# Kernel tuning notes

Measured on AMD Instinct MI355X. Metric: run time of the kernel, lower is better.

Reference implementation:

```python
import jax, jax.numpy as jnp
import numpy as np

D = 1024
EPS = 1e-5  # torch LayerNorm default


def setup_inputs() -> dict:
    key = jax.random.key(0)
    ks = jax.random.split(key, 10)
    B, S = 4, 2048
    s = 1.0 / np.sqrt(D)
    inp = {
        "x": jax.random.normal(ks[0], (B, S, D), dtype=jnp.float32),
        "gamma": jnp.ones((D,), jnp.float32),
        "beta": jnp.zeros((D,), jnp.float32),
        "Wq": jax.random.normal(ks[1], (D, D), jnp.float32) * s,
        "bq": jax.random.normal(ks[2], (D,), jnp.float32) * 0.01,
        "Wk": jax.random.normal(ks[3], (D, D), jnp.float32) * s,
        "bk": jax.random.normal(ks[4], (D,), jnp.float32) * 0.01,
        "Wv": jax.random.normal(ks[5], (D, D), jnp.float32) * s,
        "bv": jax.random.normal(ks[6], (D,), jnp.float32) * 0.01,
        "Wo": jax.random.normal(ks[7], (D, D), jnp.float32) * s,
        "bo": jax.random.normal(ks[8], (D,), jnp.float32) * 0.01,
    }
    return inp


def reference(x, gamma, beta, Wq, bq, Wk, bk, Wv, bv, Wo, bo):
    # Pre-LayerNorm
    mu = jnp.mean(x, axis=-1, keepdims=True)
    var = jnp.mean(jnp.square(x - mu), axis=-1, keepdims=True)
    xn = (x - mu) * jax.lax.rsqrt(var + EPS) * gamma + beta
    # QKV projections (torch Linear: y = x @ W.T + b)
    Q = jnp.einsum('bsd,ed->bse', xn, Wq) + bq
    K = jnp.einsum('bsd,ed->bse', xn, Wk) + bk
    V = jnp.einsum('bsd,ed->bse', xn, Wv) + bv
    # Single-head full attention, scaled by sqrt(D); dropout inactive (eval)
    scores = jnp.einsum('bqd,bkd->bqk', Q, K) / jnp.sqrt(jnp.float32(D))
    attn = jax.nn.softmax(scores, axis=-1)
    out = jnp.einsum('bqk,bkd->bqd', attn, V)
    return jnp.einsum('bsd,ed->bse', out, Wo) + bo
```

## Files before the change

kernel.cpp:

```cpp
#include <hip/hip_runtime.h>
#include <hip/hip_bf16.h>
#include <stdint.h>

typedef __attribute__((ext_vector_type(4))) float f32x4;
typedef __attribute__((ext_vector_type(8))) __bf16 bf16x8;
typedef __attribute__((ext_vector_type(8))) unsigned short ushort8;

#define DEV static __device__ __forceinline__

__device__ __align__(4096) unsigned char g_scratch[96600064];

DEV unsigned short f2bf(float f) {
  union { float f; uint32_t u; } x; x.f = f;
  uint32_t u = x.u;
  uint32_t r = (u + 0x7fffu + ((u >> 16) & 1u)) >> 16;
  return (unsigned short)r;
}
DEV float bf2f(unsigned short b) {
  union { uint32_t u; float f; } x; x.u = ((uint32_t)b) << 16;
  return x.f;
}

DEV void gload16(const void* g, void* l) {
  __builtin_amdgcn_global_load_lds((const __attribute__((address_space(1))) void*)g,
                                   (__attribute__((address_space(3))) void*)l,
                                   16, 0, 0);
}

DEV int swz(int b) { return b ^ (((b >> 7) & 7) << 4); }

DEV void gemm_core(const unsigned short* a_t, const unsigned short* b_t,
                   int ldA, int ldB, int K, unsigned short* lds, int tid,
                   const int* aOff, const int* bOff, f32x4 acc[4][4])
{
  for (int kt = 0; kt < K; kt += 64) {
#pragma unroll
    for (int i = 0; i < 4; ++i) {
      int o = i * 4096 + tid * 16;
      int p = swz(o);
      int row = p >> 7;
      int ce  = (p & 127) >> 1;
      gload16(a_t + (size_t)row * ldA + (kt + ce), (char*)lds + o);
      gload16(b_t + (size_t)row * ldB + (kt + ce), (char*)lds + 16384 + o);
    }
    __syncthreads();
#pragma unroll
    for (int h = 0; h < 2; ++h) {
      bf16x8 av[4], bv4[4];
#pragma unroll
      for (int m = 0; m < 4; ++m)
        av[m] = *(const bf16x8*)((const char*)lds + (aOff[m] ^ (h << 6)));
#pragma unroll
      for (int n = 0; n < 4; ++n)
        bv4[n] = *(const bf16x8*)((const char*)lds + (bOff[n] ^ (h << 6)));
#pragma unroll
      for (int m = 0; m < 4; ++m)
#pragma unroll
        for (int n = 0; n < 4; ++n)
          acc[m][n] = __builtin_amdgcn_mfma_f32_16x16x32_bf16(av[m], bv4[n], acc[m][n], 0, 0, 0);
    }
    __syncthreads();
  }
}

DEV void frag_offsets(int lane, int wm, int wn, int* aOff, int* bOff)
{
#pragma unroll
  for (int m = 0; m < 4; ++m) {
    int ar = wm + m * 16 + (lane & 15);
    aOff[m] = (ar * 128 + ((lane >> 4) * 16)) ^ ((ar & 7) << 4);
    int br = wn + m * 16 + (lane & 15);
    bOff[m] = ((br * 128 + ((lane >> 4) * 16)) ^ ((br & 7) << 4)) + 16384;
  }
}

DEV void tile_readback(const char* lb, unsigned short* dst, size_t ldC,
                       int wave, int lane)
{
#pragma unroll
  for (int j = 0; j < 8; ++j) {
    int row_l = wave * 32 + (lane >> 4) * 8 + j;
    int byte = (row_l * 256 + (lane & 15) * 16) ^ ((row_l & 12) << 3);
    ushort8 v = *(const ushort8*)(lb + byte);
    *(ushort8*)(dst + (size_t)row_l * ldC + (lane & 15) * 8) = v;
  }
}

__global__ __launch_bounds__(256, 4)
void g0(const unsigned short* __restrict__ wkT, const unsigned short* __restrict__ wqT,
        const unsigned short* __restrict__ woB, const unsigned short* __restrict__ wvT,
        unsigned short* __restrict__ mt, unsigned short* __restrict__ w4,
        const float* __restrict__ bq, const float* __restrict__ Wo,
        const float* __restrict__ bv, const float* __restrict__ bo,
        float* __restrict__ cvec, float* __restrict__ bb, float* __restrict__ rsm,
        const float* __restrict__ x, const float* __restrict__ gamma,
        const float* __restrict__ beta, unsigned short* __restrict__ xn)
{
  __shared__ unsigned short lds[16384];
  const int bid = blockIdx.x;
  const int tid = threadIdx.x, lane = tid & 63, wave = tid >> 6;

  if (bid >= 640) {
    const int row = bid - 640;
    float* red1 = (float*)lds;
    float* red2 = (float*)lds + 4;
    const float4 xv = ((const float4*)(x + (size_t)row * 1024))[tid];
    float s = xv.x + xv.y + xv.z + xv.w;
#pragma unroll
    for (int d = 1; d < 64; d <<= 1) s += __shfl_xor(s, d);
    if (lane == 0) red1[wave] = s;
    __syncthreads();
    const float mu = (red1[0] + red1[1] + red1[2] + red1[3]) * (1.0f / 1024.0f);
    float4 dv;
    dv.x = xv.x - mu; dv.y = xv.y - mu; dv.z = xv.z - mu; dv.w = xv.w - mu;
    float vs = dv.x * dv.x + dv.y * dv.y + dv.z * dv.z + dv.w * dv.w;
#pragma unroll
    for (int d = 1; d < 64; d <<= 1) vs += __shfl_xor(vs, d);
    if (lane == 0) red2[wave] = vs;
    __syncthreads();
    const float var = (red2[0] + red2[1] + red2[2] + red2[3]) * (1.0f / 1024.0f);
    const float rs = rsqrtf(var + 1e-5f);
    const float4 g = ((const float4*)gamma)[tid];
    const float4 b = ((const float4*)beta)[tid];
    ushort4 o;
    o.x = f2bf(dv.x * rs * g.x + b.x);
    o.y = f2bf(dv.y * rs * g.y + b.y);
    o.z = f2bf(dv.z * rs * g.z + b.z);
    o.w = f2bf(dv.w * rs * g.w + b.w);
    ((ushort4*)(xn + (size_t)row * 1024))[tid] = o;
    return;
  }

  if (bid >= 128) {
    const int b2 = bid - 128;
    if (b2 < 256) {
      if (b2 < 4) {
        const int i2 = (b2 * 256 + tid) * 2;
        ((float4*)rsm)[i2] = make_float4(0.f, 0.f, 0.f, 0.f);
        ((float4*)rsm)[i2 + 1] = make_float4(0.f, 0.f, 0.f, 0.f);
      }
      const int d = b2 * 4 + wave;
      float s = 0.f;
#pragma unroll
      for (int q = 0; q < 2; ++q) {
        ushort8 v = *(const ushort8*)(wkT + (size_t)d * 1024 + lane * 16 + q * 8);
#pragma unroll
        for (int k = 0; k < 8; ++k)
          s += bf2f(v[k]) * bq[lane * 16 + q * 8 + k];
      }
#pragma unroll
      for (int dd = 1; dd < 64; dd <<= 1) s += __shfl_xor(s, dd);
      if (lane == 0) cvec[d] = s * 0.03125f;
    } else {
      const int e = (b2 - 256) * 4 + wave;
      float s = 0.f;
#pragma unroll
      for (int q = 0; q < 4; ++q) {
        float4 a = *(const float4*)(Wo + (size_t)e * 1024 + lane * 16 + q * 4);
        float4 b = *(const float4*)(bv + lane * 16 + q * 4);
        s += a.x * b.x + a.y * b.y + a.z * b.z + a.w * b.w;
      }
#pragma unroll
      for (int dd = 1; dd < 64; dd <<= 1) s += __shfl_xor(s, dd);
      if (lane == 0) bb[e] = s + bo[e];
    }
    return;
  }

  const int z = bid >> 6;
  const int idx = bid & 63;
  const int m0 = (idx >> 3) * 128, n0 = (idx & 7) * 128;
  const int wm = (wave >> 1) * 64, wn = (wave & 1) * 64;
  int aOff[4], bOff[4];
  frag_offsets(lane, wm, wn, aOff, bOff);
  f32x4 acc[4][4] = {};
  const unsigned short* a_t = (z == 0) ? (wkT + (size_t)m0 * 1024) : (woB + (size_t)m0 * 1024);
  const unsigned short* b_t = (z == 0) ? (wqT + (size_t)n0 * 1024) : (wvT + (size_t)n0 * 1024);
  gemm_core(a_t, b_t, 1024, 1024, 1024, lds, tid, aOff, bOff, acc);

  const int r0 = (lane >> 4) * 4, cL = lane & 15;
  const float scale = (z == 0) ? 0.03125f : 1.0f;
  unsigned short* Cp = (z == 0) ? mt : w4;
#pragma unroll
  for (int n = 0; n < 4; ++n) {
    int colg = n0 + wn + n * 16 + cL;
#pragma unroll
    for (int m = 0; m < 4; ++m) {
      int rowg = m0 + wm + m * 16 + r0;
#pragma unroll
      for (int i = 0; i < 4; ++i)
        Cp[(size_t)(rowg + i) * 1024 + colg] = f2bf(acc[m][n][i] * scale);
    }
  }
}

__global__ __launch_bounds__(256, 4)
void g1(const unsigned short* __restrict__ xn, const unsigned short* __restrict__ mt,
        const unsigned short* __restrict__ w4, unsigned short* __restrict__ Z,
        unsigned short* __restrict__ yt, const float* __restrict__ cvec,
        float* __restrict__ w)
{
  __shared__ unsigned short lds[16384];
  const int tid = threadIdx.x, lane = tid & 63, wave = tid >> 6;
  const int z = blockIdx.z;

  if (z == 2) {
    const int flat = blockIdx.y * 64 + blockIdx.x;
#pragma unroll
    for (int p = 0; p < 4; ++p) {
      const int j = flat * 16 + wave * 4 + p;
      float s = 0.f;
#pragma unroll
      for (int q = 0; q < 2; ++q) {
        ushort8 v = *(const ushort8*)(xn + (size_t)j * 1024 + lane * 16 + q * 8);
#pragma unroll
        for (int k = 0; k < 8; ++k)
          s += bf2f(v[k]) * cvec[lane * 16 + q * 8 + k];
      }
#pragma unroll
      for (int d = 1; d < 64; d <<= 1) s += __shfl_xor(s, d);
      if (lane == 0) w[j] = s;
    }
    return;
  }

  const int m0 = blockIdx.x * 128, n0 = blockIdx.y * 128;
  const int wm = (wave >> 1) * 64, wn = (wave & 1) * 64;
  int aOff[4], bOff[4];
  frag_offsets(lane, wm, wn, aOff, bOff);
  f32x4 acc[4][4] = {};
  const unsigned short* b_t = ((z == 0) ? mt : w4) + (size_t)n0 * 1024;
  gemm_core(xn + (size_t)m0 * 1024, b_t, 1024, 1024, 1024, lds, tid, aOff, bOff, acc);

  const int r0 = (lane >> 4) * 4, cL = lane & 15;
  if (z == 0) {
    char* lb = (char*)lds;
#pragma unroll
    for (int n = 0; n < 4; ++n) {
      int col_l = wn + n * 16 + cL;
#pragma unroll
      for (int m = 0; m < 4; ++m)
#pragma unroll
        for (int i = 0; i < 4; ++i) {
          int row_l = wm + m * 16 + r0 + i;
          int byte = (row_l * 256 + col_l * 2) ^ ((row_l & 12) << 3);
          *(unsigned short*)(lb + byte) = f2bf(acc[m][n][i]);
        }
    }
    __syncthreads();
    tile_readback(lb, Z + (size_t)m0 * 1024 + n0, 1024, wave, lane);
  } else {
#pragma unroll
    for (int n = 0; n < 4; ++n) {
      int colg = n0 + wn + n * 16 + cL;
#pragma unroll
      for (int m = 0; m < 4; ++m) {
        int rowg = m0 + wm + m * 16 + r0;
        int bat = rowg >> 11, sdx = rowg & 2047;
        ushort4 pk;
        pk.x = f2bf(acc[m][n][0]);
        pk.y = f2bf(acc[m][n][1]);
        pk.z = f2bf(acc[m][n][2]);
        pk.w = f2bf(acc[m][n][3]);
        *(ushort4*)(yt + (size_t)bat * 2097152 + (size_t)colg * 2048 + sdx) = pk;
      }
    }
  }
}

__global__ __launch_bounds__(256, 4)
void g2(const unsigned short* __restrict__ Z, const unsigned short* __restrict__ xn,
        unsigned short* __restrict__ S, const float* __restrict__ w,
        float* __restrict__ rsum)
{
  __shared__ unsigned short lds[16384];
  const int tid = threadIdx.x, lane = tid & 63, wave = tid >> 6;
  const int z = blockIdx.z;
  const int m0 = blockIdx.x * 128, n0 = blockIdx.y * 128;
  const int wm = (wave >> 1) * 64, wn = (wave & 1) * 64;
  int aOff[4], bOff[4];
  frag_offsets(lane, wm, wn, aOff, bOff);
  f32x4 acc[4][4] = {};
  gemm_core(Z + (size_t)z * 2097152 + (size_t)m0 * 1024,
            xn + (size_t)z * 2097152 + (size_t)n0 * 1024,
            1024, 1024, 1024, lds, tid, aOff, bOff, acc);

  const int r0 = (lane >> 4) * 4, cL = lane & 15;
  char* lb = (char*)lds;
  float rs[4][4];
#pragma unroll
  for (int m = 0; m < 4; ++m)
#pragma unroll
    for (int i = 0; i < 4; ++i) rs[m][i] = 0.0f;
#pragma unroll
  for (int n = 0; n < 4; ++n) {
    int col_l = wn + n * 16 + cL;
    float wv = w[(size_t)z * 2048 + n0 + col_l];
#pragma unroll
    for (int m = 0; m < 4; ++m) {
#pragma unroll
      for (int i = 0; i < 4; ++i) {
        int row_l = wm + m * 16 + r0 + i;
        float p = __expf(acc[m][n][i] + wv - 12.0f);
        rs[m][i] += p;
        int byte = (row_l * 256 + col_l * 2) ^ ((row_l & 12) << 3);
        *(unsigned short*)(lb + byte) = f2bf(p);
      }
    }
  }
#pragma unroll
  for (int m = 0; m < 4; ++m)
#pragma unroll
    for (int i = 0; i < 4; ++i) {
      float v = rs[m][i];
      v += __shfl_xor(v, 1);
      v += __shfl_xor(v, 2);
      v += __shfl_xor(v, 4);
      v += __shfl_xor(v, 8);
      if (cL == 0)
        atomicAdd(&rsum[(size_t)z * 2048 + m0 + wm + m * 16 + r0 + i], v);
    }
  __syncthreads();
  tile_readback(lb, S + (size_t)z * 4194304 + (size_t)m0 * 2048 + n0, 2048, wave, lane);
}

__global__ __launch_bounds__(256, 4)
void g3(const unsigned short* __restrict__ S, const unsigned short* __restrict__ yt,
        float* __restrict__ out, const float* __restrict__ bb,
        const float* __restrict__ rsum)
{
  __shared__ unsigned short lds[12288];
  const int tid = threadIdx.x, lane = tid & 63, wave = tid >> 6;
  const int z = blockIdx.z;
  const int m0 = blockIdx.x * 64, n0 = blockIdx.y * 128;
  const int wm = (wave >> 1) * 32, wn = (wave & 1) * 64;

  int aOff[2], bOff[4];
#pragma unroll
  for (int m = 0; m < 2; ++m) {
    int ar = wm + m * 16 + (lane & 15);
    aOff[m] = (ar * 128 + ((lane >> 4) * 16)) ^ ((ar & 7) << 4);
  }
#pragma unroll
  for (int n = 0; n < 4; ++n) {
    int br = wn + n * 16 + (lane & 15);
    bOff[n] = ((br * 128 + ((lane >> 4) * 16)) ^ ((br & 7) << 4)) + 8192;
  }

  const unsigned short* a_t = S + (size_t)z * 4194304 + (size_t)m0 * 2048;
  const unsigned short* b_t = yt + (size_t)z * 2097152 + (size_t)n0 * 2048;

  f32x4 acc[2][4] = {};

  for (int kt = 0; kt < 2048; kt += 64) {
#pragma unroll
    for (int i = 0; i < 2; ++i) {
      int rel = i * 4096 + tid * 16;
      int p = swz(rel);
      int row = p >> 7, ce = (p & 127) >> 1;
      gload16(a_t + (size_t)row * 2048 + (kt + ce), (char*)lds + rel);
    }
#pragma unroll
    for (int i = 0; i < 4; ++i) {
      int rel = i * 4096 + tid * 16;
      int p = swz(rel);
      int row = p >> 7, ce = (p & 127) >> 1;
      gload16(b_t + (size_t)row * 2048 + (kt + ce), (char*)lds + 8192 + rel);
    }
    __syncthreads();
#pragma unroll
    for (int h = 0; h < 2; ++h) {
      bf16x8 av[2], bv4[4];
#pragma unroll
      for (int m = 0; m < 2; ++m)
        av[m] = *(const bf16x8*)((const char*)lds + (aOff[m] ^ (h << 6)));
#pragma unroll
      for (int n = 0; n < 4; ++n)
        bv4[n] = *(const bf16x8*)((const char*)lds + (bOff[n] ^ (h << 6)));
#pragma unroll
      for (int m = 0; m < 2; ++m)
#pragma unroll
        for (int n = 0; n < 4; ++n)
          acc[m][n] = __builtin_amdgcn_mfma_f32_16x16x32_bf16(av[m], bv4[n], acc[m][n], 0, 0, 0);
    }
    __syncthreads();
  }

  const int r0 = (lane >> 4) * 4, cL = lane & 15;
  float* Cp = out + (size_t)z * 2097152;
#pragma unroll
  for (int m = 0; m < 2; ++m) {
    int rowg = m0 + wm + m * 16 + r0;
#pragma unroll
    for (int i = 0; i < 4; ++i) {
      float inv = 1.0f / rsum[(size_t)z * 2048 + rowg + i];
#pragma unroll
      for (int n = 0; n < 4; ++n) {
        int colg = n0 + wn + n * 16 + cL;
        Cp[(size_t)(rowg + i) * 1024 + colg] = acc[m][n][i] * inv + bb[colg];
      }
    }
  }
}

__global__ __launch_bounds__(256)
void prep(const float* __restrict__ Wq, const float* __restrict__ Wk,
          const float* __restrict__ Wv, const float* __restrict__ Wo,
          unsigned short* __restrict__ wqT, unsigned short* __restrict__ wkT,
          unsigned short* __restrict__ wvT, unsigned short* __restrict__ woB)
{
  __shared__ float tlds[64][65];
  const int bid = blockIdx.x;
  const int tid = threadIdx.x;

  if (bid < 512) {
    const int idx = (bid * 256 + tid) * 8;
    const float4 a = *(const float4*)(Wo + idx);
    const float4 b = *(const float4*)(Wo + idx + 4);
    ushort4 r0, r1;
    r0.x = f2bf(a.x); r0.y = f2bf(a.y); r0.z = f2bf(a.z); r0.w = f2bf(a.w);
    r1.x = f2bf(b.x); r1.y = f2bf(b.y); r1.z = f2bf(b.z); r1.w = f2bf(b.w);
    *(ushort4*)(woB + idx) = r0;
    *(ushort4*)(woB + idx + 4) = r1;
    return;
  }
  {
    const int t = bid - 512;
    const int mat = t >> 8;
    const int tile = t & 255;
    const int R0 = (tile >> 4) * 64, C0 = (tile & 15) * 64;
    const float* src = (mat == 0) ? Wq : (mat == 1) ? Wk : Wv;
    unsigned short* dst = (mat == 0) ? wqT : (mat == 1) ? wkT : wvT;
#pragma unroll
    for (int p = 0; p < 4; ++p) {
      int r = p * 16 + (tid >> 4);
      int c = (tid & 15) * 4;
      float4 v = *(const float4*)(src + (size_t)(R0 + r) * 1024 + C0 + c);
      tlds[r][c + 0] = v.x; tlds[r][c + 1] = v.y;
      tlds[r][c + 2] = v.z; tlds[r][c + 3] = v.w;
    }
    __syncthreads();
    const int c = tid >> 2;
    const int chunk = tid & 3;
    ushort8 o0, o1;
#pragma unroll
    for (int k = 0; k < 8; ++k)  o0[k] = f2bf(tlds[chunk * 16 + k][c]);
#pragma unroll
    for (int k = 0; k < 8; ++k)  o1[k] = f2bf(tlds[chunk * 16 + 8 + k][c]);
    unsigned short* dp = dst + (size_t)(C0 + c) * 1024 + R0 + chunk * 16;
    *(ushort8*)(dp) = o0;
    *(ushort8*)(dp + 8) = o1;
  }
}

extern "C" void kernel_launch(void* const* d_in, const int* in_sizes, int n_in,
                              void* d_out, int out_size, void* d_ws, size_t ws_size,
                              hipStream_t stream) {
  const float* x     = (const float*)d_in[0];
  const float* gamma = (const float*)d_in[1];
  const float* beta  = (const float*)d_in[2];
  const float* Wq    = (const float*)d_in[3];
  const float* bq    = (const float*)d_in[4];
  const float* Wk    = (const float*)d_in[5];
  const float* Wv    = (const float*)d_in[7];
  const float* bv    = (const float*)d_in[8];
  const float* Wo    = (const float*)d_in[9];
  const float* bo    = (const float*)d_in[10];

  char* ws;
  if (ws_size >= (size_t)96542720) {
    ws = (char*)d_ws;
  } else {
    void* sp = nullptr;
    hipGetSymbolAddress(&sp, HIP_SYMBOL(g_scratch));
    ws = (char*)sp;
  }

  unsigned short* xn  = (unsigned short*)(ws);
  unsigned short* Z   = (unsigned short*)(ws + 16777216);
  unsigned short* yt  = (unsigned short*)(ws + 33554432);
  unsigned short* S   = (unsigned short*)(ws + 50331648);
  unsigned short* wqT = (unsigned short*)(ws + 83886080);
  unsigned short* wkT = (unsigned short*)(ws + 85983232);
  unsigned short* wvT = (unsigned short*)(ws + 88080384);
  unsigned short* woB = (unsigned short*)(ws + 90177536);
  unsigned short* mt  = (unsigned short*)(ws + 92274688);
  unsigned short* w4  = (unsigned short*)(ws + 94371840);
  float*          wv_ = (float*)(ws + 96468992);
  float*          rsm = (float*)(ws + 96501760);
  float*          bb  = (float*)(ws + 96534528);
  float*          cv  = (float*)(ws + 96538624);

  prep<<<1280, 256, 0, stream>>>(Wq, Wk, Wv, Wo, wqT, wkT, wvT, woB);
  g0<<<8832, 256, 0, stream>>>(wkT, wqT, woB, wvT, mt, w4,
                               bq, Wo, bv, bo, cv, bb, rsm,
                               x, gamma, beta, xn);
  g1<<<dim3(64, 8, 3), 256, 0, stream>>>(xn, mt, w4, Z, yt, cv, wv_);
  g2<<<dim3(16, 16, 4), 256, 0, stream>>>(Z, xn, S, wv_, rsm);
  g3<<<dim3(32, 8, 4), 256, 0, stream>>>(S, yt, (float*)d_out, bb, rsm);
}
```

Before: 152.5 us.

## Add 256x256-tile pipelined score GEMM kernel with 128KB LDS

Adds a new score-GEMM kernel that computes 256x256 output tiles with 8 waves per block. It uses 128KB of dynamic LDS, split into double-buffered A and B stages that are issued interleaved with the MFMA phases, and raises wave priority around the MFMA blocks. The aim is more data reuse per byte loaded and better overlap of global-to-LDS loads with matrix math. The exp, row-sum and atomic epilogue is kept the same as before. In exchange, occupancy drops to one block per CU and only 256 blocks are launched, and the old kernel remains as a fallback if the LDS attribute cannot be set.

New measurement: 162.3 us. 6.4% more time.

```diff
diff --git a/kernel.cpp b/kernel.cpp
--- a/kernel.cpp
+++ b/kernel.cpp
@@ -266,6 +266,152 @@
       }
     }
   }
+}
+
+__global__ __launch_bounds__(512, 1)
+void g2f(const unsigned short* __restrict__ Z, const unsigned short* __restrict__ xn,
+         unsigned short* __restrict__ S, const float* __restrict__ w,
+         float* __restrict__ rsum)
+{
+  extern __shared__ char lds[];
+  const int tid  = threadIdx.x;
+  const int lane = tid & 63;
+  const int wave = tid >> 6;
+  const int wr = wave >> 2;
+  const int wc = wave & 3;
+  const int z  = blockIdx.z;
+  const int m0 = blockIdx.x * 256;
+  const int n0 = blockIdx.y * 256;
+  const int K  = 1024, ldA = 1024, ldB = 1024;
+  const unsigned short* a_t = Z  + (size_t)z * 2097152 + (size_t)m0 * ldA;
+  const unsigned short* b_t = xn + (size_t)z * 2097152 + (size_t)n0 * ldB;
+
+  const int so0 = tid * 16;        const int sp0 = swz(so0);
+  const int sr0 = sp0 >> 7, sc0 = (sp0 & 127) >> 1;
+  const int so1 = 8192 + tid * 16; const int sp1 = swz(so1);
+  const int sr1 = sp1 >> 7, sc1 = (sp1 & 127) >> 1;
+
+  int aoff[8];
+#pragma unroll
+  for (int mi = 0; mi < 8; ++mi) {
+    int r = mi * 16 + (lane & 15);
+    aoff[mi] = (r * 128 + ((lane >> 4) * 16)) ^ ((r & 7) << 4);
+  }
+  int boff[4];
+#pragma unroll
+  for (int ni = 0; ni < 4; ++ni) {
+    int r = (wc & 1) * 64 + ni * 16 + (lane & 15);
+    boff[ni] = (r * 128 + ((lane >> 4) * 16)) ^ ((r & 7) << 4);
+  }
+
+  f32x4 acc[8][4] = {};
+
+  auto STAGE = [&](int base, const unsigned short* src, int ld, int kc) {
+    gload16(src + sr0 * ld + kc + sc0, lds + base + so0);
+    gload16(src + sr1 * ld + kc + sc1, lds + base + so1);
+  };
+
+  const int NI = K >> 7;
+  STAGE(32768,  b_t,             ldB, 0);
+  STAGE(49152,  b_t + 128 * ldB, ldB, 0);
+  STAGE(0,      a_t,             ldA, 0);
+  STAGE(16384,  a_t + 128 * ldA, ldA, 0);
+  STAGE(98304,  b_t,             ldB, 64);
+  STAGE(114688, b_t + 128 * ldB, ldB, 64);
+  asm volatile("s_waitcnt vmcnt(4)" ::: "memory");
+  __builtin_amdgcn_s_barrier();
+
+  for (int it = 0; it < NI; ++it) {
+    const int kA1 = it * 128 + 64;
+    int kn  = it * 128 + 128; if (kn  > K - 64) kn  = K - 64;
+    int kn2 = it * 128 + 192; if (kn2 > K - 64) kn2 = K - 64;
+#pragma unroll
+    for (int c = 0; c < 2; ++c) {
+      const char* aB = lds + c * 65536 + wr * 16384;
+      const char* bB = lds + c * 65536 + 32768 + (wc >> 1) * 16384;
+      bf16x8 bfr[4][2];
+#pragma unroll
+      for (int q = 0; q < 4; ++q) {
+        const int p = c * 4 + q;
+        if (q == 0) {
+#pragma unroll
+          for (int ni = 0; ni < 4; ++ni)
+#pragma unroll
+            for (int h = 0; h < 2; ++h)
+              bfr[ni][h] = *(const bf16x8*)(bB + (boff[ni] ^ (h << 6)));
+        }
+        bf16x8 afr[2][2];
+#pragma unroll
+        for (int m2 = 0; m2 < 2; ++m2)
+#pragma unroll
+          for (int h = 0; h < 2; ++h)
+            afr[m2][h] = *(const bf16x8*)(aB + (aoff[q * 2 + m2] ^ (h << 6)));
+        if (p == 0)      STAGE(65536,  a_t,             ldA, kA1);
+        else if (p == 1) STAGE(81920,  a_t + 128 * ldA, ldA, kA1);
+        else if (p == 2) STAGE(32768,  b_t,             ldB, kn);
+        else if (p == 3) STAGE(49152,  b_t + 128 * ldB, ldB, kn);
+        else if (p == 4) STAGE(0,      a_t,             ldA, kn);
+        else if (p == 5) STAGE(16384,  a_t + 128 * ldA, ldA, kn);
+        else if (p == 6) STAGE(98304,  b_t,             ldB, kn2);
+        else             STAGE(114688, b_t + 128 * ldB, ldB, kn2);
+        if (q == 0) asm volatile("s_waitcnt lgkmcnt(8)" ::: "memory");
+        __builtin_amdgcn_s_barrier();
+        asm volatile("s_waitcnt lgkmcnt(0)" ::: "memory");
+        __builtin_amdgcn_s_setprio(1);
+#pragma unroll
+        for (int h = 0; h < 2; ++h)
+#pragma unroll
+          for (int ni = 0; ni < 4; ++ni)
+#pragma unroll
+            for (int m2 = 0; m2 < 2; ++m2)
+              acc[q * 2 + m2][ni] = __builtin_amdgcn_mfma_f32_16x16x32_bf16(
+                  afr[m2][h], bfr[ni][h], acc[q * 2 + m2][ni], 0, 0, 0);
+        __builtin_amdgcn_s_setprio(0);
+        if (q == 3) asm volatile("s_waitcnt vmcnt(4)" ::: "memory");
+        __builtin_amdgcn_s_barrier();
+      }
+    }
+  }
+
+  const int r0 = (lane >> 4) * 4;
+  const int cL = lane & 15;
+  const int wrow = m0 + wr * 128;
+  const int wcol = n0 + wc * 64;
+  unsigned short* Cp = S + (size_t)z * 4194304;
+
+  float rs[8][4];
+#pragma unroll
+  for (int mi = 0; mi < 8; ++mi)
+#pragma unroll
+    for (int i = 0; i < 4; ++i) rs[mi][i] = 0.0f;
+
+#pragma unroll
+  for (int ni = 0; ni < 4; ++ni) {
+    int colg = wcol + ni * 16 + cL;
+    float wv = w[(size_t)z * 2048 + colg];
+#pragma unroll
+    for (int mi = 0; mi < 8; ++mi) {
+      int rowg = wrow + mi * 16 + r0;
+#pragma unroll
+      for (int i = 0; i < 4; ++i) {
+        float p = __expf(acc[mi][ni][i] + wv - 12.0f);
+        rs[mi][i] += p;
+        Cp[(size_t)(rowg + i) * 2048 + colg] = f2bf(p);
+      }
+    }
+  }
+#pragma unroll
+  for (int mi = 0; mi < 8; ++mi)
+#pragma unroll
+    for (int i = 0; i < 4; ++i) {
+      float v = rs[mi][i];
+      v += __shfl_xor(v, 1);
+      v += __shfl_xor(v, 2);
+      v += __shfl_xor(v, 4);
+      v += __shfl_xor(v, 8);
+      if (cL == 0)
+        atomicAdd(&rsum[(size_t)z * 2048 + wrow + mi * 16 + r0 + i], v);
+    }
 }
 
 __global__ __launch_bounds__(256, 4)
@@ -491,11 +637,19 @@
   float*          bb  = (float*)(ws + 96534528);
   float*          cv  = (float*)(ws + 96538624);
 
+  int use256 =
+      (hipFuncSetAttribute(reinterpret_cast<const void*>(&g2f),
+                           hipFuncAttributeMaxDynamicSharedMemorySize,
+                           131072) == hipSuccess);
+
   prep<<<1280, 256, 0, stream>>>(Wq, Wk, Wv, Wo, wqT, wkT, wvT, woB);
   g0<<<8832, 256, 0, stream>>>(wkT, wqT, woB, wvT, mt, w4,
                                bq, Wo, bv, bo, cv, bb, rsm,
                                x, gamma, beta, xn);
   g1<<<dim3(64, 8, 3), 256, 0, stream>>>(xn, mt, w4, Z, yt, cv, wv_);
-  g2<<<dim3(16, 16, 4), 256, 0, stream>>>(Z, xn, S, wv_, rsm);
+  if (use256)
+    g2f<<<dim3(8, 8, 4), 512, 131072, stream>>>(Z, xn, S, wv_, rsm);
+  else
+    g2<<<dim3(16, 16, 4), 256, 0, stream>>>(Z, xn, S, wv_, rsm);
   g3<<<dim3(32, 8, 4), 256, 0, stream>>>(S, yt, (float*)d_out, bb, rsm);
 }
```
